# Kernel tuning notes

Hardware: AMD Instinct MI355X
Metric: run time of the kernel (lower is better)

The kernel has to match this reference:

```python
import jax, jax.numpy as jnp
import numpy as np

H, KVH, D, HID = 32, 32, 128, 4096
THETA = 10000.0
EPS = 1e-5


def setup_inputs() -> dict:
    key = jax.random.key(0)
    ks = jax.random.split(key, 7)
    T = 2048
    return {
        "positions": jnp.arange(T, dtype=jnp.int32),
        "hidden_states": jax.random.normal(ks[0], (T, HID), dtype=jnp.float32),
        "w_qkv": jax.random.normal(ks[1], ((H + 2 * KVH) * D, HID), dtype=jnp.float32) * 0.02,
        "w_o": jax.random.normal(ks[2], (HID, H * D), dtype=jnp.float32) * 0.02,
        "q_norm_w": jax.random.uniform(ks[3], (H, D), dtype=jnp.float32),
        "q_norm_b": jax.random.normal(ks[4], (H, D), dtype=jnp.float32) * 0.02,
        "k_norm_w": jax.random.uniform(ks[5], (KVH, D), dtype=jnp.float32),
        "k_norm_b": jax.random.normal(ks[6], (KVH, D), dtype=jnp.float32) * 0.02,
    }


def _per_head_ln(x, w, b):
    # x: [T, H, D]; layer_norm over last dim without affine, then *w + b (per head)
    mu = jnp.mean(x, axis=-1, keepdims=True)
    var = jnp.mean(jnp.square(x - mu), axis=-1, keepdims=True)
    xn = (x - mu) * jax.lax.rsqrt(var + EPS)
    return xn * w + b


def _rope(x, positions):
    # neox-style rotate-half RoPE; x: [T, H, D]
    half = D // 2
    inv_freq = 1.0 / (THETA ** (jnp.arange(0, D, 2, dtype=jnp.float32) / D))  # [D/2]
    freqs = positions.astype(jnp.float32)[:, None] * inv_freq  # [T, D/2]
    cos = jnp.cos(freqs)[:, None, :]  # [T, 1, D/2]
    sin = jnp.sin(freqs)[:, None, :]
    x1, x2 = x[..., :half], x[..., half:]
    return jnp.concatenate([x1 * cos - x2 * sin, x2 * cos + x1 * sin], axis=-1)


def reference(positions, hidden_states, w_qkv, w_o, q_norm_w, q_norm_b, k_norm_w, k_norm_b):
    T = hidden_states.shape[0]
    qkv = hidden_states @ w_qkv.T  # [T, (H+2*KVH)*D]
    q, k, v = jnp.split(qkv, [H * D, (H + KVH) * D], axis=-1)
    q = q.reshape(T, H, D)
    k = k.reshape(T, KVH, D)
    v = v.reshape(T, KVH, D)
    q = _per_head_ln(q, q_norm_w, q_norm_b)
    k = _per_head_ln(k, k_norm_w, k_norm_b)
    q = _rope(q, positions)
    k = _rope(k, positions)
    scale = D ** -0.5
    scores = jnp.einsum("qhd,khd->hqk", q, k) * scale  # [H, T, T]
    causal = jnp.tril(jnp.ones((T, T), dtype=bool))
    scores = jnp.where(causal, scores, jnp.finfo(scores.dtype).min)
    probs = jax.nn.softmax(scores, axis=-1)
    attn = jnp.einsum("hqk,khd->qhd", probs, v).reshape(T, H * D)
    return attn @ w_o.T  # [T, HID]
```

## Files before the change

### kernel.cpp

```cpp
#include <hip/hip_runtime.h>
#include <cstdint>

typedef unsigned short u16;
typedef __attribute__((ext_vector_type(8))) __bf16 bf16x8;
typedef __attribute__((ext_vector_type(4))) float f32x4;

__device__ __forceinline__ u16 f2bf(float f) {
  unsigned int u = __builtin_bit_cast(unsigned int, f);
  unsigned int r = (u + 0x7fffu + ((u >> 16) & 1u)) >> 16;
  return (u16)r;
}

__device__ __forceinline__ void gload16(const u16* g, u16* l) {
  __builtin_amdgcn_global_load_lds((const __attribute__((address_space(1))) void*)g,
                                   (__attribute__((address_space(3))) void*)l, 16, 0, 0);
}

__device__ __forceinline__ int swz64i(int row, int col) {
  return row * 64 + (((col & 0x38) ^ ((row & 7) << 3)) | (col & 7));
}
__device__ __forceinline__ int swz128i(int row, int col) {
  return row * 128 + (((col & 0x78) ^ ((row & 7) << 3)) | (col & 7));
}

__global__ __launch_bounds__(256) void cvt_bf16_kernel(const float* __restrict__ in,
                                                       u16* __restrict__ out, long n4) {
  long i = (long)blockIdx.x * 256 + threadIdx.x;
  long stride = (long)gridDim.x * 256;
  const float4* in4 = (const float4*)in;
  uint2* out2 = (uint2*)out;
  for (long k = i; k < n4; k += stride) {
    float4 v = in4[k];
    uint2 o;
    o.x = (unsigned int)f2bf(v.x) | ((unsigned int)f2bf(v.y) << 16);
    o.y = (unsigned int)f2bf(v.z) | ((unsigned int)f2bf(v.w) << 16);
    out2[k] = o;
  }
}

__global__ __launch_bounds__(512, 2) void gemm256(const u16* __restrict__ A,
                                                  const u16* __restrict__ B,
                                                  float* __restrict__ C,
                                                  int Ndim, int Kdim) {
  extern __shared__ __align__(16) u16 lds[];
  const int tid = threadIdx.x;
  const int lane = tid & 63, wave = tid >> 6;
  const int wr = wave >> 2, wc = wave & 3;
  const int l15 = lane & 15, l4 = lane >> 4;
  const int gx = gridDim.x;
  int lin = blockIdx.y * gx + blockIdx.x;
  const int xcd = lin & 7, ii = lin >> 3;
  const int bx = xcd * (gx >> 3) + (ii >> 3), by = ii & 7;
  const long arow = (long)by * 256, brow = (long)bx * 128;
  const int NT = Kdim >> 6;

  const int rowt = tid >> 3;
  const int koff = ((tid & 7) ^ (rowt & 7)) * 8;
  const u16* gA[4];
  const u16* gB[2];
  #pragma unroll
  for (int r = 0; r < 4; ++r) gA[r] = A + (size_t)(arow + rowt + r * 64) * Kdim + koff;
  #pragma unroll
  for (int r = 0; r < 2; ++r) gB[r] = B + (size_t)(brow + rowt + r * 64) * Kdim + koff;

  auto STA = [&](int u) {
    u16* d = lds + (u % 3) * 16384 + tid * 8;
    #pragma unroll
    for (int r = 0; r < 4; ++r) gload16(gA[r] + (size_t)u * 64, d + r * 4096);
  };
  auto STB = [&](int u) {
    u16* d = lds + 49152 + (u & 1) * 8192 + tid * 8;
    #pragma unroll
    for (int r = 0; r < 2; ++r) gload16(gB[r] + (size_t)u * 64, d + r * 4096);
  };

  bf16x8 af[4][2], bfr[2][2];
  f32x4 acc[8][2] = {};
  int cks[2];
  #pragma unroll
  for (int kc = 0; kc < 2; ++kc) cks[kc] = (((kc * 4 + l4) ^ (l15 & 7)) * 8);

  auto LDA = [&](int u, int mh) {
    const u16* base = lds + (u % 3) * 16384 + (wr * 128 + mh * 64 + l15) * 64;
    #pragma unroll
    for (int m = 0; m < 4; ++m)
      #pragma unroll
      for (int kc = 0; kc < 2; ++kc)
        af[m][kc] = *(const bf16x8*)(base + m * 1024 + cks[kc]);
  };
  auto LDB = [&](int u) {
    const u16* base = lds + 49152 + (u & 1) * 8192 + (wc * 32 + l15) * 64;
    #pragma unroll
    for (int n = 0; n < 2; ++n)
      #pragma unroll
      for (int kc = 0; kc < 2; ++kc)
        bfr[n][kc] = *(const bf16x8*)(base + n * 1024 + cks[kc]);
  };
  auto MM = [&](int mh) {
    #pragma unroll
    for (int kc = 0; kc < 2; ++kc)
      #pragma unroll
      for (int m = 0; m < 4; ++m)
        #pragma unroll
        for (int n = 0; n < 2; ++n)
          acc[mh * 4 + m][n] =
            __builtin_amdgcn_mfma_f32_16x16x32_bf16(af[m][kc], bfr[n][kc],
                                                    acc[mh * 4 + m][n], 0, 0, 0);
  };

#define PH_BEGIN() do { __builtin_amdgcn_s_barrier();                         \
    asm volatile("s_waitcnt lgkmcnt(0)" ::: "memory");                        \
    __builtin_amdgcn_sched_barrier(0);                                        \
    __builtin_amdgcn_s_setprio(1); } while (0)

  STA(0); STB(0); STA(1); STB(1);
  asm volatile("s_waitcnt vmcnt(6)" ::: "memory");
  __builtin_amdgcn_s_barrier();

  for (int u = 0; u < NT; ++u) {
    LDA(u, 0); LDB(u);
    if (u + 2 < NT) STA(u + 2);
    PH_BEGIN(); MM(0);
    __builtin_amdgcn_s_setprio(0);
    __builtin_amdgcn_s_barrier();
    LDA(u, 1);
    if (u + 2 < NT) STB(u + 2);
    PH_BEGIN(); MM(1);
    __builtin_amdgcn_s_setprio(0);
    if (u + 2 < NT) { asm volatile("s_waitcnt vmcnt(6)" ::: "memory"); }
    else if (u + 1 < NT) { asm volatile("s_waitcnt vmcnt(0)" ::: "memory"); }
    __builtin_amdgcn_s_barrier();
  }
#undef PH_BEGIN

  #pragma unroll
  for (int M = 0; M < 8; ++M)
    #pragma unroll
    for (int n = 0; n < 2; ++n)
      #pragma unroll
      for (int j = 0; j < 4; ++j) {
        long r = arow + wr * 128 + M * 16 + l4 * 4 + j;
        long c = brow + wc * 32 + n * 16 + l15;
        C[r * Ndim + c] = acc[M][n][j];
      }
}

__global__ __launch_bounds__(256) void ln_rope_kernel(
    const float* __restrict__ qkv, const int* __restrict__ pos,
    const float* __restrict__ qw, const float* __restrict__ qb2,
    const float* __restrict__ kw, const float* __restrict__ kb2,
    u16* __restrict__ qo, u16* __restrict__ ko, u16* __restrict__ vo, int T) {
  const int hh = blockIdx.x;
  const int t = blockIdx.y * 4 + (threadIdx.x >> 6);
  const int lane = threadIdx.x & 63;
  const float* src = qkv + (size_t)t * 12288 + hh * 128;
  float x1 = src[lane], x2 = src[lane + 64];
  if (hh >= 64) {
    u16* dst = vo + ((size_t)(hh - 64) * T + t) * 128;
    dst[lane] = f2bf(x1); dst[lane + 64] = f2bf(x2);
    return;
  }
  float s = x1 + x2;
  #pragma unroll
  for (int off = 32; off; off >>= 1) s += __shfl_xor(s, off);
  float mu = s * (1.0f / 128.0f);
  float d1 = x1 - mu, d2 = x2 - mu;
  float vs = d1 * d1 + d2 * d2;
  #pragma unroll
  for (int off = 32; off; off >>= 1) vs += __shfl_xor(vs, off);
  float rstd = rsqrtf(vs * (1.0f / 128.0f) + 1e-5f);
  bool isq = hh < 32;
  int hl = isq ? hh : hh - 32;
  const float* w = (isq ? qw : kw) + hl * 128;
  const float* b = (isq ? qb2 : kb2) + hl * 128;
  float y1 = d1 * rstd * w[lane] + b[lane];
  float y2 = d2 * rstd * w[lane + 64] + b[lane + 64];
  float p = (float)pos[t];
  float invf = exp2f((float)lane * (-13.287712379549449f / 64.0f));
  float fr = p * invf;
  float sn, cs;
  __sincosf(fr, &sn, &cs);
  float o1 = y1 * cs - y2 * sn;
  float o2 = y2 * cs + y1 * sn;
  if (isq) {
    const float sc = 0.08838834764831845f;
    o1 *= sc; o2 *= sc;
    u16* dst = qo + ((size_t)hl * T + t) * 128;
    dst[lane] = f2bf(o1); dst[lane + 64] = f2bf(o2);
  } else {
    u16* dst = ko + ((size_t)hl * T + t) * 128;
    dst[lane] = f2bf(o1); dst[lane + 64] = f2bf(o2);
  }
}

__global__ __launch_bounds__(256, 2) void flash_kernel(
    const u16* __restrict__ qb, const u16* __restrict__ kb,
    const u16* __restrict__ vb, u16* __restrict__ attn, int T) {
  __shared__ __align__(16) u16 Ks[64 * 128];
  __shared__ __align__(16) u16 Vt[128 * 64];
  __shared__ __align__(16) u16 Ps[4][32 * 64];
  const int tid = threadIdx.x;
  const int lane = tid & 63, wave = tid >> 6;
  const int l15 = lane & 15, l4 = lane >> 4;
  const int h = blockIdx.y;
  const int qbase = blockIdx.x * 128;
  const int qrow0 = qbase + wave * 32;
  const u16* Q  = qb + (size_t)h * T * 128;
  const u16* Kp = kb + (size_t)h * T * 128;
  const u16* Vp = vb + (size_t)h * T * 128;
  const int rK0 = tid >> 4, d8k = (tid & 15) * 8;

  bf16x8 qf[2][4];
  #pragma unroll
  for (int mi = 0; mi < 2; ++mi)
    #pragma unroll
    for (int kc = 0; kc < 4; ++kc)
      qf[mi][kc] = *(const bf16x8*)&Q[(size_t)(qrow0 + mi * 16 + l15) * 128 + kc * 32 + l4 * 8];

  float m_st[2][4], l_st[2][4];
  f32x4 o[2][8] = {};
  #pragma unroll
  for (int mi = 0; mi < 2; ++mi)
    #pragma unroll
    for (int j = 0; j < 4; ++j) { m_st[mi][j] = -1e30f; l_st[mi][j] = 0.0f; }

  const int ntile = (qbase + 128) / 64;
  uint4 kr[4], vr[4];
  #pragma unroll
  for (int c = 0; c < 4; ++c) {
    kr[c] = *(const uint4*)&Kp[(size_t)(rK0 + 16 * c) * 128 + d8k];
    vr[c] = *(const uint4*)&Vp[(size_t)lane * 128 + (wave + 4 * c) * 8];
  }
  for (int kt = 0; kt < ntile; ++kt) {
    const int kbase = kt * 64;
    #pragma unroll
    for (int c = 0; c < 4; ++c) {
      *(uint4*)&Ks[swz128i(rK0 + 16 * c, d8k)] = kr[c];
      const u16* pv = (const u16*)&vr[c];
      int dv = (wave + 4 * c) * 8;
      #pragma unroll
      for (int j = 0; j < 8; ++j) Vt[swz64i(dv + j, lane)] = pv[j];
    }
    __syncthreads();
    if (kt + 1 < ntile) {
      const int nb = kbase + 64;
      #pragma unroll
      for (int c = 0; c < 4; ++c) {
        kr[c] = *(const uint4*)&Kp[(size_t)(nb + rK0 + 16 * c) * 128 + d8k];
        vr[c] = *(const uint4*)&Vp[(size_t)(nb + lane) * 128 + (wave + 4 * c) * 8];
      }
    }
    if (kbase <= qrow0 + 31) {
      f32x4 s[2][4] = {};
      __builtin_amdgcn_s_setprio(1);
      #pragma unroll
      for (int kc = 0; kc < 4; ++kc)
        #pragma unroll
        for (int nj = 0; nj < 4; ++nj) {
          bf16x8 kf = *(const bf16x8*)&Ks[swz128i(nj * 16 + l15, kc * 32 + l4 * 8)];
          #pragma unroll
          for (int mi = 0; mi < 2; ++mi)
            s[mi][nj] = __builtin_amdgcn_mfma_f32_16x16x32_bf16(qf[mi][kc], kf, s[mi][nj], 0, 0, 0);
        }
      __builtin_amdgcn_s_setprio(0);
      if (kbase + 63 > qrow0) {
        #pragma unroll
        for (int mi = 0; mi < 2; ++mi)
          #pragma unroll
          for (int nj = 0; nj < 4; ++nj)
            #pragma unroll
            for (int j = 0; j < 4; ++j) {
              int r = qrow0 + mi * 16 + l4 * 4 + j;
              int cc = kbase + nj * 16 + l15;
              if (cc > r) s[mi][nj][j] = -1e30f;
            }
      }
      float vmax[2][4];
      float dmax = -1e30f;
      #pragma unroll
      for (int mi = 0; mi < 2; ++mi)
        #pragma unroll
        for (int j = 0; j < 4; ++j) {
          float v = fmaxf(fmaxf(s[mi][0][j], s[mi][1][j]), fmaxf(s[mi][2][j], s[mi][3][j]));
          #pragma unroll
          for (int off = 1; off < 16; off <<= 1) v = fmaxf(v, __shfl_xor(v, off));
          vmax[mi][j] = v;
          dmax = fmaxf(dmax, v - m_st[mi][j]);
        }
      if (!__all(dmax <= 8.0f)) {
        #pragma unroll
        for (int mi = 0; mi < 2; ++mi)
          #pragma unroll
          for (int j = 0; j < 4; ++j) {
            float mn = fmaxf(m_st[mi][j], vmax[mi][j]);
            float scl = __expf(m_st[mi][j] - mn);
            m_st[mi][j] = mn;
            l_st[mi][j] *= scl;
            #pragma unroll
            for (int nf = 0; nf < 8; ++nf) o[mi][nf][j] *= scl;
          }
      }
      #pragma unroll
      for (int mi = 0; mi < 2; ++mi) {
        float sum[4] = {0.f, 0.f, 0.f, 0.f};
        #pragma unroll
        for (int nj = 0; nj < 4; ++nj)
          #pragma unroll
          for (int j = 0; j < 4; ++j) {
            float p = __expf(s[mi][nj][j] - m_st[mi][j]);
            s[mi][nj][j] = p;
            sum[j] += p;
          }
        #pragma unroll
        for (int j = 0; j < 4; ++j) {
          #pragma unroll
          for (int off = 1; off < 16; off <<= 1) sum[j] += __shfl_xor(sum[j], off);
          l_st[mi][j] += sum[j];
        }
        #pragma unroll
        for (int nj = 0; nj < 4; ++nj)
          #pragma unroll
          for (int j = 0; j < 4; ++j)
            Ps[wave][swz64i(mi * 16 + l4 * 4 + j, nj * 16 + l15)] = f2bf(s[mi][nj][j]);
      }
      asm volatile("s_waitcnt lgkmcnt(0)" ::: "memory");
      __builtin_amdgcn_sched_barrier(0);
      __builtin_amdgcn_s_setprio(1);
      #pragma unroll
      for (int mi = 0; mi < 2; ++mi)
        #pragma unroll
        for (int kc = 0; kc < 2; ++kc) {
          bf16x8 pf = *(const bf16x8*)&Ps[wave][swz64i(mi * 16 + l15, kc * 32 + l4 * 8)];
          #pragma unroll
          for (int nf = 0; nf < 8; ++nf) {
            bf16x8 vf = *(const bf16x8*)&Vt[swz64i(nf * 16 + l15, kc * 32 + l4 * 8)];
            o[mi][nf] = __builtin_amdgcn_mfma_f32_16x16x32_bf16(pf, vf, o[mi][nf], 0, 0, 0);
          }
        }
      __builtin_amdgcn_s_setprio(0);
    }
    __syncthreads();
  }
  #pragma unroll
  for (int mi = 0; mi < 2; ++mi) {
    float rl[4];
    #pragma unroll
    for (int j = 0; j < 4; ++j) rl[j] = 1.0f / l_st[mi][j];
    #pragma unroll
    for (int nf = 0; nf < 8; ++nf)
      #pragma unroll
      for (int j = 0; j < 4; ++j) {
        int r = qrow0 + mi * 16 + l4 * 4 + j;
        int cc = h * 128 + nf * 16 + l15;
        attn[(size_t)r * 4096 + cc] = f2bf(o[mi][nf][j] * rl[j]);
      }
  }
}

extern "C" void kernel_launch(void* const* d_in, const int* in_sizes, int n_in,
                              void* d_out, int out_size, void* d_ws, size_t ws_size,
                              hipStream_t stream) {
  const int* positions = (const int*)d_in[0];
  const float* hidden  = (const float*)d_in[1];
  const float* w_qkv   = (const float*)d_in[2];
  const float* w_o     = (const float*)d_in[3];
  const float* qnw     = (const float*)d_in[4];
  const float* qnb     = (const float*)d_in[5];
  const float* knw     = (const float*)d_in[6];
  const float* knb     = (const float*)d_in[7];
  float* out = (float*)d_out;

  const int T = in_sizes[0];
  const int HID = 4096, NQKV = 12288, H = 32;

  char* ws = (char*)d_ws;
  u16* hid_bf  = (u16*)ws;
  u16* wreg    = (u16*)(ws + (size_t)T * HID * 2);
  float* qkv_f = (float*)(ws + (size_t)T * HID * 2 + (size_t)NQKV * HID * 2);

  u16* q_bf  = wreg;
  u16* k_bf  = q_bf + (size_t)H * T * 128;
  u16* v_bf  = k_bf + (size_t)H * T * 128;
  u16* at_bf = v_bf + (size_t)H * T * 128;
  u16* wo_bf = at_bf + (size_t)T * 4096;

  hipFuncSetAttribute(reinterpret_cast<const void*>(&gemm256),
                      hipFuncAttributeMaxDynamicSharedMemorySize, 131072);

  cvt_bf16_kernel<<<2048, 256, 0, stream>>>(hidden, hid_bf, (long)T * HID / 4);
  cvt_bf16_kernel<<<4096, 256, 0, stream>>>(w_qkv, wreg, (long)NQKV * HID / 4);
  gemm256<<<dim3(NQKV / 128, T / 256), 512, 131072, stream>>>(hid_bf, wreg, qkv_f, NQKV, HID);
  ln_rope_kernel<<<dim3(96, T / 4), 256, 0, stream>>>(qkv_f, positions, qnw, qnb, knw, knb,
                                                      q_bf, k_bf, v_bf, T);
  cvt_bf16_kernel<<<2048, 256, 0, stream>>>(w_o, wo_bf, (long)HID * HID / 4);
  flash_kernel<<<dim3(T / 128, H), 256, 0, stream>>>(q_bf, k_bf, v_bf, at_bf, T);
  gemm256<<<dim3(HID / 128, T / 256), 512, 131072, stream>>>(at_bf, wo_bf, out, HID, HID);
}
```

Baseline: 559.5 us.

## Use 256x256 tile GEMM with quadrant-phased MFMA schedule for QKV projection

```diff
diff --git a/kernel.cpp b/kernel.cpp
--- a/kernel.cpp
+++ b/kernel.cpp
@@ -36,6 +36,139 @@
     o.y = (unsigned int)f2bf(v.z) | ((unsigned int)f2bf(v.w) << 16);
     out2[k] = o;
   }
+}
+
+__global__ __launch_bounds__(512, 2) void gemm256sq(const u16* __restrict__ A,
+                                                    const u16* __restrict__ B,
+                                                    float* __restrict__ C,
+                                                    int Ndim, int Kdim) {
+  extern __shared__ __align__(16) u16 lds[];
+  const int tid = threadIdx.x;
+  const int lane = tid & 63, wave = tid >> 6;
+  const int wr = wave >> 2, wc = wave & 3;
+  const int l15 = lane & 15, l4 = lane >> 4;
+  const int gx = gridDim.x;
+  int lin = blockIdx.y * gx + blockIdx.x;
+  const int xcd = lin & 7, ii = lin >> 3;
+  const int bx = xcd * (gx >> 3) + (ii >> 3), by = ii & 7;
+  const long arow = (long)by * 256, brow = (long)bx * 256;
+  const int NT = Kdim >> 6, NI = NT >> 1;
+
+  const int rowt = tid >> 3;
+  const int koff = ((tid & 7) ^ (rowt & 7)) * 8;
+  const u16* gA[2][2];
+  const u16* gB[2][2];
+  #pragma unroll
+  for (int h = 0; h < 2; ++h)
+    #pragma unroll
+    for (int g = 0; g < 2; ++g) {
+      gA[h][g] = A + (size_t)(arow + h * 128 + g * 64 + rowt) * Kdim + koff;
+      gB[h][g] = B + (size_t)(brow + h * 128 + g * 64 + rowt) * Kdim + koff;
+    }
+
+  auto STA = [&](int u, int h, int b) {
+    u16* d = lds + b * 16384 + h * 8192 + tid * 8;
+    gload16(gA[h][0] + (size_t)u * 64, d);
+    gload16(gA[h][1] + (size_t)u * 64, d + 4096);
+  };
+  auto STB = [&](int u, int h, int b) {
+    u16* d = lds + 32768 + b * 16384 + h * 8192 + tid * 8;
+    gload16(gB[h][0] + (size_t)u * 64, d);
+    gload16(gB[h][1] + (size_t)u * 64, d + 4096);
+  };
+
+  bf16x8 af[4][2], bfr0[2][2], bfr1[2][2];
+  f32x4 acc[8][4] = {};
+  int cks[2];
+  #pragma unroll
+  for (int kc = 0; kc < 2; ++kc) cks[kc] = (((kc * 4 + l4) ^ (l15 & 7)) * 8);
+
+  auto LDA = [&](int b, int mh) {
+    const u16* base = lds + b * 16384 + (wr * 128 + mh * 64 + l15) * 64;
+    #pragma unroll
+    for (int m = 0; m < 4; ++m)
+      #pragma unroll
+      for (int kc = 0; kc < 2; ++kc)
+        af[m][kc] = *(const bf16x8*)(base + m * 1024 + cks[kc]);
+  };
+  auto LDB = [&](int b, int nh, bf16x8 (*bf)[2]) {
+    const u16* base = lds + 32768 + b * 16384 + (wc * 64 + nh * 32 + l15) * 64;
+    #pragma unroll
+    for (int n = 0; n < 2; ++n)
+      #pragma unroll
+      for (int kc = 0; kc < 2; ++kc)
+        bf[n][kc] = *(const bf16x8*)(base + n * 1024 + cks[kc]);
+  };
+  auto MMQ = [&](int mh, int nh, bf16x8 (*bf)[2]) {
+    #pragma unroll
+    for (int kc = 0; kc < 2; ++kc)
+      #pragma unroll
+      for (int m = 0; m < 4; ++m)
+        #pragma unroll
+        for (int n = 0; n < 2; ++n)
+          acc[mh * 4 + m][nh * 2 + n] =
+            __builtin_amdgcn_mfma_f32_16x16x32_bf16(af[m][kc], bf[n][kc],
+                                                    acc[mh * 4 + m][nh * 2 + n], 0, 0, 0);
+  };
+
+#define PH_BEGIN() do { __builtin_amdgcn_s_barrier();                         \
+    asm volatile("s_waitcnt lgkmcnt(0)" ::: "memory");                        \
+    __builtin_amdgcn_sched_barrier(0);                                        \
+    __builtin_amdgcn_s_setprio(1); } while (0)
+#define PH_END() do { __builtin_amdgcn_s_setprio(0);                          \
+    __builtin_amdgcn_s_barrier(); } while (0)
+
+  STA(0, 0, 0); STA(0, 1, 0); STB(0, 0, 0); STB(0, 1, 0);
+  STA(1, 0, 1);
+  asm volatile("s_waitcnt vmcnt(2)" ::: "memory");
+  __builtin_amdgcn_s_barrier();
+
+  for (int i = 0; i < NI; ++i) {
+    const int t0 = 2 * i, t1 = 2 * i + 1;
+    LDA(0, 0); LDB(0, 0, bfr0);
+    STA(t1, 1, 1);
+    PH_BEGIN(); MMQ(0, 0, bfr0); PH_END();
+    LDB(0, 1, bfr1);
+    STB(t1, 0, 1);
+    PH_BEGIN(); MMQ(0, 1, bfr1); PH_END();
+    LDA(0, 1);
+    STB(t1, 1, 1);
+    PH_BEGIN(); MMQ(1, 1, bfr1); PH_END();
+    if (t0 + 2 < NT) STA(t0 + 2, 0, 0);
+    PH_BEGIN(); MMQ(1, 0, bfr0);
+    __builtin_amdgcn_s_setprio(0);
+    if (t0 + 2 < NT) { asm volatile("s_waitcnt vmcnt(2)" ::: "memory"); }
+    else             { asm volatile("s_waitcnt vmcnt(0)" ::: "memory"); }
+    __builtin_amdgcn_s_barrier();
+    LDA(1, 0); LDB(1, 0, bfr0);
+    if (t0 + 2 < NT) STA(t0 + 2, 1, 0);
+    PH_BEGIN(); MMQ(0, 0, bfr0); PH_END();
+    LDB(1, 1, bfr1);
+    if (t0 + 2 < NT) STB(t0 + 2, 0, 0);
+    PH_BEGIN(); MMQ(0, 1, bfr1); PH_END();
+    LDA(1, 1);
+    if (t0 + 2 < NT) STB(t0 + 2, 1, 0);
+    PH_BEGIN(); MMQ(1, 1, bfr1); PH_END();
+    if (t1 + 2 < NT) STA(t1 + 2, 0, 1);
+    PH_BEGIN(); MMQ(1, 0, bfr0);
+    __builtin_amdgcn_s_setprio(0);
+    if (t1 + 2 < NT) { asm volatile("s_waitcnt vmcnt(2)" ::: "memory"); }
+    else             { asm volatile("s_waitcnt vmcnt(0)" ::: "memory"); }
+    __builtin_amdgcn_s_barrier();
+  }
+#undef PH_BEGIN
+#undef PH_END
+
+  #pragma unroll
+  for (int M = 0; M < 8; ++M)
+    #pragma unroll
+    for (int n2 = 0; n2 < 4; ++n2)
+      #pragma unroll
+      for (int j = 0; j < 4; ++j) {
+        long r = arow + wr * 128 + (M >> 2) * 64 + (M & 3) * 16 + l4 * 4 + j;
+        long c = brow + wc * 64 + n2 * 16 + l15;
+        C[r * Ndim + c] = acc[M][n2][j];
+      }
 }
 
 __global__ __launch_bounds__(512, 2) void gemm256(const u16* __restrict__ A,
@@ -384,12 +517,14 @@
   u16* at_bf = v_bf + (size_t)H * T * 128;
   u16* wo_bf = at_bf + (size_t)T * 4096;
 
+  hipFuncSetAttribute(reinterpret_cast<const void*>(&gemm256sq),
+                      hipFuncAttributeMaxDynamicSharedMemorySize, 131072);
   hipFuncSetAttribute(reinterpret_cast<const void*>(&gemm256),
                       hipFuncAttributeMaxDynamicSharedMemorySize, 131072);
 
   cvt_bf16_kernel<<<2048, 256, 0, stream>>>(hidden, hid_bf, (long)T * HID / 4);
   cvt_bf16_kernel<<<4096, 256, 0, stream>>>(w_qkv, wreg, (long)NQKV * HID / 4);
-  gemm256<<<dim3(NQKV / 128, T / 256), 512, 131072, stream>>>(hid_bf, wreg, qkv_f, NQKV, HID);
+  gemm256sq<<<dim3(NQKV / 256, T / 256), 512, 131072, stream>>>(hid_bf, wreg, qkv_f, NQKV, HID);
   ln_rope_kernel<<<dim3(96, T / 4), 256, 0, stream>>>(qkv_f, positions, qnw, qnb, knw, knb,
                                                       q_bf, k_bf, v_bf, T);
   cvt_bf16_kernel<<<2048, 256, 0, stream>>>(w_o, wo_bf, (long)HID * HID / 4);
```

Result: no change. 568.9 us (+1.7%).
